# Performance work log

Hardware: AMD Instinct MI355X
Metric: run time of the kernel (lower is better)

Reference implementation:

```python
import jax, jax.numpy as jnp
import numpy as np

# Quantization constants (mirror the torch module's __init__ kwargs)
INPUT_SCALE = 0.0625          # q_in: Quantize(input_scale, 0, qint8)
SCORE_SCALE = 0.00390625      # npu_matmul output_scale for scores (1/256)
PROB_SCALE = 0.00048828125    # q_probs: Quantize(prob_scale, 0, qint8) (1/2048)
I8_MIN, I8_MAX = -128, 127
I16_MIN, I16_MAX = -32768, 32767

D, K, M, N = 256, 256, 256, 65536  # w1:[K,D], x:[D,N], w2:[M,K]


def quantize_i8(x, scale):
    # torch Quantize: round-half-to-even(x/scale) + zp(=0), clamp to int8
    return jnp.clip(jnp.round(x / scale), I8_MIN, I8_MAX).astype(jnp.int8)


def npu_matmul_i16(w_i8, x_i8):
    acc = jnp.matmul(w_i8.astype(jnp.int32), x_i8.astype(jnp.int32))
    return jnp.clip(acc, I16_MIN, I16_MAX).astype(jnp.int16)


def setup_inputs() -> dict:
    key = jax.random.key(0)
    k1, k2, k3 = jax.random.split(key, 3)
    x = jax.random.normal(k1, (D, N), dtype=jnp.float32)
    # weights are pre-quantized int8 values stored as float32 (as in the torch module)
    w1 = jax.random.randint(k2, (K, D), -16, 16).astype(jnp.float32)
    w2 = jax.random.randint(k3, (M, K), -16, 16).astype(jnp.float32)
    return {"x": x, "w1": w1, "w2": w2}


def reference(x, w1, w2):
    x_q = quantize_i8(x, INPUT_SCALE)                       # [D, N] int8
    scores_q = npu_matmul_i16(w1.astype(jnp.int8), x_q)     # [K, N] int16 (quantized, scale=SCORE_SCALE)
    scores = scores_q.astype(jnp.float32) * SCORE_SCALE     # dequantize
    probs = jax.nn.softmax(scores, axis=0)                  # softmax over dim 0
    q_probs = quantize_i8(probs, PROB_SCALE)                # [K, N] int8
    out = npu_matmul_i16(w2.astype(jnp.int8), q_probs)      # [M, N] int16
    return out
```

## Files before the change

kernel.cpp:

```cpp
#include <hip/hip_runtime.h>

typedef int   int4v   __attribute__((ext_vector_type(4)));
typedef float float4v __attribute__((ext_vector_type(4)));

#define N_DIM 65536

__device__ __forceinline__ int quant8(float v) {
    int q = (int)rintf(v);
    q = q > 127 ? 127 : q;
    q = q < -128 ? -128 : q;
    return q;
}

__device__ __forceinline__ int clamp16(int s) {
    s = s > 32767 ? 32767 : s;
    s = s < -32768 ? -32768 : s;
    return s;
}

__device__ __forceinline__ unsigned int qpack(float4v v) {
    int q0 = quant8(v.x * 16.0f);
    int q1 = quant8(v.y * 16.0f);
    int q2 = quant8(v.z * 16.0f);
    int q3 = quant8(v.w * 16.0f);
    return (unsigned int)((q0 & 0xff) | ((q1 & 0xff) << 8) |
                          ((q2 & 0xff) << 16) | ((q3 & 0xff) << 24));
}

__device__ __forceinline__ float fexp2(float a) {
    float r;
    asm("v_exp_f32 %0, %1" : "=v"(r) : "v"(a));
    return r;
}

__global__ __launch_bounds__(256) void quant_weights(const float* __restrict__ w1,
                                                     const float* __restrict__ w2,
                                                     unsigned char* __restrict__ w1q,
                                                     unsigned char* __restrict__ w2q) {
    int idx = blockIdx.x * 256 + threadIdx.x;
    const float* src;
    unsigned char* dst;
    int off;
    if (idx < 16384) { src = w1; dst = w1q; off = idx * 4; }
    else             { src = w2; dst = w2q; off = (idx - 16384) * 4; }
    float4v f = *reinterpret_cast<const float4v*>(src + off);
    unsigned int dw = (unsigned int)(((int)f.x & 0xff) | (((int)f.y & 0xff) << 8) |
                                     (((int)f.z & 0xff) << 16) | (((int)f.w & 0xff) << 24));
    *reinterpret_cast<unsigned int*>(dst + off) = dw;
}

__global__ __launch_bounds__(512, 3) void qdq_main(const float* __restrict__ x,
                                                   const unsigned char* __restrict__ w1q,
                                                   const unsigned char* __restrict__ w2q,
                                                   int* __restrict__ out) {
    __shared__ unsigned char xq[8192];
    __shared__ unsigned char pq[8192];
    __shared__ int   mb[8][32];
    __shared__ float sb[8][32];

    const int tid  = threadIdx.x;
    const int wv   = tid >> 6;
    const int lane = tid & 63;
    const int c    = lane & 15;
    const int g    = lane >> 4;

    const int rsub = lane >> 3;
    const int cg   = lane & 7;
    const int R    = rsub & 3;
    const unsigned int sel1 = (R & 1) ? 0x03070206u : 0x05010400u;
    const unsigned int sel2 = (R & 2) ? 0x07060302u : 0x01000504u;
    const int colsel = (0x3120 >> (R * 4)) & 0xF;
    const int n_t = cg * 4 + colsel;
    const int qb  = rsub & 4;

    int4v a1f[2][4], a2f[2][4];
    {
        const unsigned char* a1 = w1q + (size_t)(wv * 32 + c) * 256 + g * 16;
        const unsigned char* a2 = w2q + (size_t)(wv * 32 + c) * 256 + g * 16;
        #pragma unroll
        for (int rt = 0; rt < 2; ++rt)
            #pragma unroll
            for (int kk = 0; kk < 4; ++kk) {
                a1f[rt][kk] = *reinterpret_cast<const int4v*>(a1 + rt * 4096 + kk * 64);
                a2f[rt][kk] = *reinterpret_cast<const int4v*>(a2 + rt * 4096 + kk * 64);
            }
    }

    const int colstart = blockIdx.x * 256;
    const float* xpb = x + (size_t)(wv * 32 + rsub) * N_DIM + cg * 4;

    float4v raw[4];
    #pragma unroll
    for (int i = 0; i < 4; ++i)
        raw[i] = *reinterpret_cast<const float4v*>(xpb + (size_t)i * (8 * N_DIM) + colstart);

    const float C = 0.0056355275034725134f;

    for (int it = 0; it < 8; ++it) {
        const int col0 = colstart + it * 32;

        unsigned int Wq[4];
        #pragma unroll
        for (int i = 0; i < 4; ++i) Wq[i] = qpack(raw[i]);
        if (it < 7) {
            #pragma unroll
            for (int i = 0; i < 4; ++i)
                raw[i] = *reinterpret_cast<const float4v*>(
                    xpb + (size_t)i * (8 * N_DIM) + (col0 + 32));
        }

        #pragma unroll
        for (int i = 0; i < 4; ++i) {
            unsigned int t = (unsigned int)__shfl_xor((int)Wq[i], 8);
            unsigned int Q = __builtin_amdgcn_perm(t, Wq[i], sel1);
            unsigned int u = (unsigned int)__shfl_xor((int)Q, 16);
            unsigned int F = __builtin_amdgcn_perm(Q, u, sel2);
            const int dbase = wv * 32 + i * 8 + qb;
            *reinterpret_cast<unsigned int*>(
                xq + n_t * 256 + (dbase ^ ((n_t & 15) << 4))) = F;
        }
        __syncthreads();

        int4v bq[2][4];
        #pragma unroll
        for (int t2 = 0; t2 < 2; ++t2)
            #pragma unroll
            for (int kk = 0; kk < 4; ++kk)
                bq[t2][kk] = *reinterpret_cast<const int4v*>(
                    xq + (t2 * 16 + c) * 256 + ((kk * 64 + g * 16) ^ (c << 4)));

        unsigned int scA[4], scB[4];
        int imA = -(1 << 30), imB = -(1 << 30);
        #pragma unroll
        for (int rt = 0; rt < 2; ++rt) {
            int4v accA = {0, 0, 0, 0}, accB = {0, 0, 0, 0};
            #pragma unroll
            for (int kk = 0; kk < 4; ++kk) {
                accA = __builtin_amdgcn_mfma_i32_16x16x64_i8(a1f[rt][kk], bq[0][kk], accA, 0, 0, 0);
                accB = __builtin_amdgcn_mfma_i32_16x16x64_i8(a1f[rt][kk], bq[1][kk], accB, 0, 0, 0);
            }
            {
                const int s0 = clamp16(accA[0]), s1 = clamp16(accA[1]);
                const int s2 = clamp16(accA[2]), s3 = clamp16(accA[3]);
                int m01 = s0 > s1 ? s0 : s1, m23 = s2 > s3 ? s2 : s3;
                int m = m01 > m23 ? m01 : m23;
                imA = imA > m ? imA : m;
                scA[2 * rt]     = (unsigned int)((s0 & 0xffff) | (s1 << 16));
                scA[2 * rt + 1] = (unsigned int)((s2 & 0xffff) | (s3 << 16));
            }
            {
                const int s0 = clamp16(accB[0]), s1 = clamp16(accB[1]);
                const int s2 = clamp16(accB[2]), s3 = clamp16(accB[3]);
                int m01 = s0 > s1 ? s0 : s1, m23 = s2 > s3 ? s2 : s3;
                int m = m01 > m23 ? m01 : m23;
                imB = imB > m ? imB : m;
                scB[2 * rt]     = (unsigned int)((s0 & 0xffff) | (s1 << 16));
                scB[2 * rt + 1] = (unsigned int)((s2 & 0xffff) | (s3 << 16));
            }
        }

        {
            int o = __shfl_xor(imA, 16); imA = imA > o ? imA : o;
            o = __shfl_xor(imA, 32);     imA = imA > o ? imA : o;
            o = __shfl_xor(imB, 16);     imB = imB > o ? imB : o;
            o = __shfl_xor(imB, 32);     imB = imB > o ? imB : o;
        }
        if (g == 0) mb[wv][c] = imA;
        else if (g == 1) mb[wv][16 + c] = imB;
        __syncthreads();
        int gmA = mb[0][c], gmB = mb[0][16 + c];
        #pragma unroll
        for (int j = 1; j < 8; ++j) {
            int a = mb[j][c], b = mb[j][16 + c];
            gmA = gmA > a ? gmA : a;
            gmB = gmB > b ? gmB : b;
        }

        float sA = 0.0f, sB = 0.0f;
        #pragma unroll
        for (int i = 0; i < 4; ++i) {
            sA += fexp2((float)((int)(short)(scA[i] & 0xffffu) - gmA) * C);
            sA += fexp2((float)(((int)scA[i] >> 16) - gmA) * C);
            sB += fexp2((float)((int)(short)(scB[i] & 0xffffu) - gmB) * C);
            sB += fexp2((float)(((int)scB[i] >> 16) - gmB) * C);
        }
        sA += __shfl_xor(sA, 16); sA += __shfl_xor(sA, 32);
        sB += __shfl_xor(sB, 16); sB += __shfl_xor(sB, 32);
        if (g == 0) sb[wv][c] = sA;
        else if (g == 1) sb[wv][16 + c] = sB;
        __syncthreads();
        float gsA = 0.0f, gsB = 0.0f;
        #pragma unroll
        for (int j = 0; j < 8; ++j) { gsA += sb[j][c]; gsB += sb[j][16 + c]; }
        const float qsA = 2048.0f / gsA;
        const float qsB = 2048.0f / gsB;

        #pragma unroll
        for (int rt = 0; rt < 2; ++rt) {
            const int koff = wv * 32 + rt * 16 + g * 4;
            {
                const unsigned int w0 = scA[2 * rt], w1 = scA[2 * rt + 1];
                int q0 = (int)rintf(fexp2((float)((int)(short)(w0 & 0xffffu) - gmA) * C) * qsA);
                int q1 = (int)rintf(fexp2((float)(((int)w0 >> 16) - gmA) * C) * qsA);
                int q2 = (int)rintf(fexp2((float)((int)(short)(w1 & 0xffffu) - gmA) * C) * qsA);
                int q3 = (int)rintf(fexp2((float)(((int)w1 >> 16) - gmA) * C) * qsA);
                q0 = q0 > 127 ? 127 : q0;
                q1 = q1 > 127 ? 127 : q1;
                q2 = q2 > 127 ? 127 : q2;
                q3 = q3 > 127 ? 127 : q3;
                *reinterpret_cast<unsigned int*>(
                    pq + c * 256 + (koff ^ (c << 4))) =
                    (unsigned int)(q0 | (q1 << 8) | (q2 << 16) | (q3 << 24));
            }
            {
                const unsigned int w0 = scB[2 * rt], w1 = scB[2 * rt + 1];
                int q0 = (int)rintf(fexp2((float)((int)(short)(w0 & 0xffffu) - gmB) * C) * qsB);
                int q1 = (int)rintf(fexp2((float)(((int)w0 >> 16) - gmB) * C) * qsB);
                int q2 = (int)rintf(fexp2((float)((int)(short)(w1 & 0xffffu) - gmB) * C) * qsB);
                int q3 = (int)rintf(fexp2((float)(((int)w1 >> 16) - gmB) * C) * qsB);
                q0 = q0 > 127 ? 127 : q0;
                q1 = q1 > 127 ? 127 : q1;
                q2 = q2 > 127 ? 127 : q2;
                q3 = q3 > 127 ? 127 : q3;
                *reinterpret_cast<unsigned int*>(
                    pq + (16 + c) * 256 + (koff ^ (c << 4))) =
                    (unsigned int)(q0 | (q1 << 8) | (q2 << 16) | (q3 << 24));
            }
        }
        __syncthreads();

        int4v b2[2][4];
        #pragma unroll
        for (int t2 = 0; t2 < 2; ++t2)
            #pragma unroll
            for (int kk = 0; kk < 4; ++kk)
                b2[t2][kk] = *reinterpret_cast<const int4v*>(
                    pq + (t2 * 16 + c) * 256 + ((kk * 64 + g * 16) ^ (c << 4)));

        #pragma unroll
        for (int rt = 0; rt < 2; ++rt) {
            int4v accA = {0, 0, 0, 0}, accB = {0, 0, 0, 0};
            #pragma unroll
            for (int kk = 0; kk < 4; ++kk) {
                accA = __builtin_amdgcn_mfma_i32_16x16x64_i8(a2f[rt][kk], b2[0][kk], accA, 0, 0, 0);
                accB = __builtin_amdgcn_mfma_i32_16x16x64_i8(a2f[rt][kk], b2[1][kk], accB, 0, 0, 0);
            }
            #pragma unroll
            for (int r = 0; r < 4; ++r) {
                const size_t rowoff =
                    (size_t)(wv * 32 + rt * 16 + g * 4 + r) * N_DIM + col0;
                out[rowoff + c]      = clamp16(accA[r]);
                out[rowoff + 16 + c] = clamp16(accB[r]);
            }
        }
    }
}

extern "C" void kernel_launch(void* const* d_in, const int* in_sizes, int n_in,
                              void* d_out, int out_size, void* d_ws, size_t ws_size,
                              hipStream_t stream) {
    const float* x  = (const float*)d_in[0];
    const float* w1 = (const float*)d_in[1];
    const float* w2 = (const float*)d_in[2];
    int* out = (int*)d_out;

    unsigned char* w1q = (unsigned char*)d_ws;
    unsigned char* w2q = w1q + 65536;

    quant_weights<<<128, 256, 0, stream>>>(w1, w2, w1q, w2q);
    qdq_main<<<256, 512, 0, stream>>>(x, w1q, w2q, out);
}
```

Baseline: 42.43 us.

## Use online-softmax rescaling to drop a barrier and cache exponentials

Replaces the two-barrier softmax (global max, then sum) with a single barrier. Each wave computes exponentials against its local max and publishes both max and partial sum, and these are rescaled after one sync. The per-element exponentials are kept in registers so they are not recomputed for quantization. W2 fragments are reloaded from global memory each iteration instead of being held in registers, which lowers register pressure at the cost of extra loads. Output stores become nontemporal. The reordered floating-point arithmetic could shift int8 rounding at boundaries relative to the reference.

```diff
diff --git a/kernel.cpp b/kernel.cpp
--- a/kernel.cpp
+++ b/kernel.cpp
@@ -73,18 +73,16 @@
     const int n_t = cg * 4 + colsel;
     const int qb  = rsub & 4;
 
-    int4v a1f[2][4], a2f[2][4];
+    int4v a1f[2][4];
     {
         const unsigned char* a1 = w1q + (size_t)(wv * 32 + c) * 256 + g * 16;
-        const unsigned char* a2 = w2q + (size_t)(wv * 32 + c) * 256 + g * 16;
         #pragma unroll
         for (int rt = 0; rt < 2; ++rt)
             #pragma unroll
-            for (int kk = 0; kk < 4; ++kk) {
+            for (int kk = 0; kk < 4; ++kk)
                 a1f[rt][kk] = *reinterpret_cast<const int4v*>(a1 + rt * 4096 + kk * 64);
-                a2f[rt][kk] = *reinterpret_cast<const int4v*>(a2 + rt * 4096 + kk * 64);
-            }
     }
+    const unsigned char* a2 = w2q + (size_t)(wv * 32 + c) * 256 + g * 16;
 
     const int colstart = blockIdx.x * 256;
     const float* xpb = x + (size_t)(wv * 32 + rsub) * N_DIM + cg * 4;
@@ -167,43 +165,54 @@
         }
         if (g == 0) mb[wv][c] = imA;
         else if (g == 1) mb[wv][16 + c] = imB;
-        __syncthreads();
-        int gmA = mb[0][c], gmB = mb[0][16 + c];
-        #pragma unroll
-        for (int j = 1; j < 8; ++j) {
-            int a = mb[j][c], b = mb[j][16 + c];
-            gmA = gmA > a ? gmA : a;
-            gmB = gmB > b ? gmB : b;
-        }
-
+        float eA[8], eB[8];
         float sA = 0.0f, sB = 0.0f;
         #pragma unroll
         for (int i = 0; i < 4; ++i) {
-            sA += fexp2((float)((int)(short)(scA[i] & 0xffffu) - gmA) * C);
-            sA += fexp2((float)(((int)scA[i] >> 16) - gmA) * C);
-            sB += fexp2((float)((int)(short)(scB[i] & 0xffffu) - gmB) * C);
-            sB += fexp2((float)(((int)scB[i] >> 16) - gmB) * C);
+            eA[2 * i]     = fexp2((float)((int)(short)(scA[i] & 0xffffu) - imA) * C);
+            eA[2 * i + 1] = fexp2((float)(((int)scA[i] >> 16) - imA) * C);
+            sA += eA[2 * i] + eA[2 * i + 1];
+            eB[2 * i]     = fexp2((float)((int)(short)(scB[i] & 0xffffu) - imB) * C);
+            eB[2 * i + 1] = fexp2((float)(((int)scB[i] >> 16) - imB) * C);
+            sB += eB[2 * i] + eB[2 * i + 1];
         }
         sA += __shfl_xor(sA, 16); sA += __shfl_xor(sA, 32);
         sB += __shfl_xor(sB, 16); sB += __shfl_xor(sB, 32);
         if (g == 0) sb[wv][c] = sA;
         else if (g == 1) sb[wv][16 + c] = sB;
+
+        int4v a2f[2][4];
+        #pragma unroll
+        for (int rt = 0; rt < 2; ++rt)
+            #pragma unroll
+            for (int kk = 0; kk < 4; ++kk)
+                a2f[rt][kk] = *reinterpret_cast<const int4v*>(a2 + rt * 4096 + kk * 64);
         __syncthreads();
+
+        int gmA = -(1 << 30), gmB = -(1 << 30);
+        #pragma unroll
+        for (int j = 0; j < 8; ++j) {
+            int a = mb[j][c], b = mb[j][16 + c];
+            gmA = gmA > a ? gmA : a;
+            gmB = gmB > b ? gmB : b;
+        }
         float gsA = 0.0f, gsB = 0.0f;
         #pragma unroll
-        for (int j = 0; j < 8; ++j) { gsA += sb[j][c]; gsB += sb[j][16 + c]; }
-        const float qsA = 2048.0f / gsA;
-        const float qsB = 2048.0f / gsB;
+        for (int j = 0; j < 8; ++j) {
+            gsA += sb[j][c]      * fexp2((float)(mb[j][c] - gmA) * C);
+            gsB += sb[j][16 + c] * fexp2((float)(mb[j][16 + c] - gmB) * C);
+        }
+        const float qsA = (2048.0f / gsA) * fexp2((float)(imA - gmA) * C);
+        const float qsB = (2048.0f / gsB) * fexp2((float)(imB - gmB) * C);
 
         #pragma unroll
         for (int rt = 0; rt < 2; ++rt) {
             const int koff = wv * 32 + rt * 16 + g * 4;
             {
-                const unsigned int w0 = scA[2 * rt], w1 = scA[2 * rt + 1];
-                int q0 = (int)rintf(fexp2((float)((int)(short)(w0 & 0xffffu) - gmA) * C) * qsA);
-                int q1 = (int)rintf(fexp2((float)(((int)w0 >> 16) - gmA) * C) * qsA);
-                int q2 = (int)rintf(fexp2((float)((int)(short)(w1 & 0xffffu) - gmA) * C) * qsA);
-                int q3 = (int)rintf(fexp2((float)(((int)w1 >> 16) - gmA) * C) * qsA);
+                int q0 = (int)rintf(eA[4 * rt + 0] * qsA);
+                int q1 = (int)rintf(eA[4 * rt + 1] * qsA);
+                int q2 = (int)rintf(eA[4 * rt + 2] * qsA);
+                int q3 = (int)rintf(eA[4 * rt + 3] * qsA);
                 q0 = q0 > 127 ? 127 : q0;
                 q1 = q1 > 127 ? 127 : q1;
                 q2 = q2 > 127 ? 127 : q2;
@@ -213,11 +222,10 @@
                     (unsigned int)(q0 | (q1 << 8) | (q2 << 16) | (q3 << 24));
             }
             {
-                const unsigned int w0 = scB[2 * rt], w1 = scB[2 * rt + 1];
-                int q0 = (int)rintf(fexp2((float)((int)(short)(w0 & 0xffffu) - gmB) * C) * qsB);
-                int q1 = (int)rintf(fexp2((float)(((int)w0 >> 16) - gmB) * C) * qsB);
-                int q2 = (int)rintf(fexp2((float)((int)(short)(w1 & 0xffffu) - gmB) * C) * qsB);
-                int q3 = (int)rintf(fexp2((float)(((int)w1 >> 16) - gmB) * C) * qsB);
+                int q0 = (int)rintf(eB[4 * rt + 0] * qsB);
+                int q1 = (int)rintf(eB[4 * rt + 1] * qsB);
+                int q2 = (int)rintf(eB[4 * rt + 2] * qsB);
+                int q3 = (int)rintf(eB[4 * rt + 3] * qsB);
                 q0 = q0 > 127 ? 127 : q0;
                 q1 = q1 > 127 ? 127 : q1;
                 q2 = q2 > 127 ? 127 : q2;
@@ -249,8 +257,8 @@
             for (int r = 0; r < 4; ++r) {
                 const size_t rowoff =
                     (size_t)(wv * 32 + rt * 16 + g * 4 + r) * N_DIM + col0;
-                out[rowoff + c]      = clamp16(accA[r]);
-                out[rowoff + 16 + c] = clamp16(accB[r]);
+                __builtin_nontemporal_store(clamp16(accA[r]), &out[rowoff + c]);
+                __builtin_nontemporal_store(clamp16(accB[r]), &out[rowoff + 16 + c]);
             }
         }
     }
```

Result: slower. 43.96 us (+3.6%).
